# Performance work log

Measured on AMD Instinct MI355X. Metric: run time of the kernel, lower is better.

Reference implementation:

```python
import jax, jax.numpy as jnp
import numpy as np

S, B, E = 4096, 2, 1024
H = 8
WIN = 256  # one-sided window w; band width = 2*w+1


def _band_scores(q, k_pad, seq_len, band):
    # q: (B,S,H,D), k_pad: (B,S+2w,H,D). Returns (B,S,H,band) banded QK^T.
    def f(o):
        ks = jax.lax.dynamic_slice_in_dim(k_pad, o, seq_len, axis=1)
        return jnp.einsum('bshd,bshd->bsh', q, ks)
    s = jax.lax.map(f, jnp.arange(band))  # (band,B,S,H)
    return jnp.moveaxis(s, 0, -1)          # (B,S,H,band)


def _band_av(probs, v_pad, seq_len, band):
    # probs: (B,S,H,band), v_pad: (B,S+2w,H,D) zero-padded (out-of-range keys
    # contribute zero vectors, matching diagonaled_mm's internal masking).
    bsz, _, heads, _ = probs.shape
    d = v_pad.shape[-1]
    def body(carry, o):
        vs = jax.lax.dynamic_slice_in_dim(v_pad, o, seq_len, axis=1)
        p = jax.lax.dynamic_slice_in_dim(probs, o, 1, axis=3)  # (B,S,H,1)
        return carry + p * vs, None
    init = jnp.zeros((bsz, seq_len, heads, d), probs.dtype)
    out, _ = jax.lax.scan(body, init, jnp.arange(band))
    return out


def setup_inputs() -> dict:
    key = jax.random.key(0)
    ks = jax.random.split(key, 7)
    val = jax.random.normal(ks[0], (S, B, E), dtype=jnp.float32)
    Wq = jax.random.normal(ks[1], (E, E), dtype=jnp.float32) * 0.02
    bq = jax.random.normal(ks[2], (E,), dtype=jnp.float32) * 0.02
    Wk = jax.random.normal(ks[3], (E, E), dtype=jnp.float32) * 0.02
    bk = jax.random.normal(ks[4], (E,), dtype=jnp.float32) * 0.02
    Wv = jax.random.normal(ks[5], (E, E), dtype=jnp.float32) * 0.02
    bv = jax.random.normal(ks[6], (E,), dtype=jnp.float32) * 0.02
    return {"val": val, "Wq": Wq, "bq": bq, "Wk": Wk, "bk": bk, "Wv": Wv, "bv": bv}


def reference(val, Wq, bq, Wk, bk, Wv, bv):
    seq_len, bsz, embed = val.shape
    heads, w = H, WIN
    d = embed // heads
    band = 2 * w + 1
    x = jnp.swapaxes(val, 0, 1)  # (B,S,E), matches val.transpose(0,1)
    scale = 1.0 / np.sqrt(d)
    q = (x @ Wq.T + bq) * scale
    k = x @ Wk.T + bk
    v = x @ Wv.T + bv
    # Faithful to torch: .view(seq_len, bsz, H, D) on a (bsz, seq_len, E)
    # contiguous tensor reinterprets memory (a scramble when B != S), then
    # transpose(0,1). jnp.reshape on row-major matches torch .view exactly.
    mq = jnp.swapaxes(q.reshape(seq_len, bsz, heads, d), 0, 1)  # (B,S,H,D)
    mk = jnp.swapaxes(k.reshape(seq_len, bsz, heads, d), 0, 1)
    mv = jnp.swapaxes(v.reshape(seq_len, bsz, heads, d), 0, 1)
    k_pad = jnp.pad(mk, ((0, 0), (w, w), (0, 0), (0, 0)))  # zero pad => padding=0 scores
    v_pad = jnp.pad(mv, ((0, 0), (w, w), (0, 0), (0, 0)))
    scores = _band_scores(mq, k_pad, seq_len, band)  # (B,S,H,2w+1)
    # No masking before softmax (faithful: padding=0 entries enter softmax as 0)
    probs = jax.nn.softmax(scores, axis=-1)
    # dropout in eval mode (training=False) is identity
    attn = _band_av(probs, v_pad, seq_len, band)  # (B,S,H,D)
    out = jnp.swapaxes(attn, 0, 1).reshape(seq_len, bsz, embed)
    return out
```

## Files before the change

### kernel.cpp

```cpp
#include <hip/hip_runtime.h>
#include <stdint.h>

#define SEQ   4096
#define EMB   1024
#define HD    128
#define WIN   256
#define MROWS 8192

typedef unsigned short u16;
typedef unsigned long long u64;
typedef __bf16 v8bf  __attribute__((ext_vector_type(8)));
typedef float  v4f   __attribute__((ext_vector_type(4)));
typedef u16    v8u16 __attribute__((ext_vector_type(8)));

__device__ __forceinline__ u16 f2bf(float f) {
  uint32_t u = __builtin_bit_cast(uint32_t, f);
  u += 0x7FFFu + ((u >> 16) & 1u);
  return (u16)(u >> 16);
}
__device__ __forceinline__ void gl_lds16(const u16* g, u16* l) {
  __builtin_amdgcn_global_load_lds((const __attribute__((address_space(1))) void*)g,
                                   (__attribute__((address_space(3))) void*)l,
                                   16, 0, 0);
}

__global__ __launch_bounds__(256)
void cvt_f32_bf16(const float* __restrict__ val,
                  const float* __restrict__ Wq,
                  const float* __restrict__ Wk,
                  const float* __restrict__ Wv,
                  u16* __restrict__ valbf, u16* __restrict__ Wbf)
{
  const int seg = blockIdx.y;
  const float* src; u16* dst; int nblk;
  if (seg == 0)      { src = val; dst = valbf;              nblk = 4096; }
  else if (seg == 1) { src = Wq;  dst = Wbf;                nblk = 512;  }
  else if (seg == 2) { src = Wk;  dst = Wbf + (1u << 20);   nblk = 512;  }
  else               { src = Wv;  dst = Wbf + (2u << 20);   nblk = 512;  }
  if ((int)blockIdx.x >= nblk) return;
  const int t = blockIdx.x * 256 + threadIdx.x;
  float4 a = ((const float4*)src)[2 * t];
  float4 b = ((const float4*)src)[2 * t + 1];
  v8u16 o;
  o[0] = f2bf(a.x); o[1] = f2bf(a.y); o[2] = f2bf(a.z); o[3] = f2bf(a.w);
  o[4] = f2bf(b.x); o[5] = f2bf(b.y); o[6] = f2bf(b.z); o[7] = f2bf(b.w);
  ((v8u16*)dst)[t] = o;
}

__global__ __launch_bounds__(256, 3)
void qkv_gemm(const u16* __restrict__ valbf, const u16* __restrict__ Wbf,
              const float* __restrict__ bq, const float* __restrict__ bk,
              const float* __restrict__ bv,
              u16* __restrict__ Qb, u16* __restrict__ Kb, u16* __restrict__ VTg)
{
  __shared__ __align__(16) u16 As[128 * 64];
  __shared__ __align__(16) u16 Bs[128 * 64];

  const int tid  = threadIdx.x;
  const int lane = tid & 63;
  const int w    = tid >> 6;
  const int quad = lane >> 4;
  const int lq   = lane & 15;
  const int wm   = w >> 1, wn = w & 1;

  const int bn = blockIdx.x;
  const int bm = blockIdx.y;

  const int seg = bn >> 3;
  const u16*   Wsel = Wbf + (size_t)seg * EMB * EMB;
  const float* bsel = seg == 0 ? bq : (seg == 1 ? bk : bv);
  const int nseg0 = (bn & 7) * 128;

  const u16* arow[4];
  const u16* brow[4];
#pragma unroll
  for (int call = 0; call < 4; ++call) {
    int c  = call * 256 + w * 64 + lane;
    int m  = c >> 3;
    int qs = c & 7;
    int q  = qs ^ (m & 7);
    int a2 = bm * 128 + m;
    int aa = 2 * (a2 & 4095) + (a2 >> 12);
    int grow = (aa & 4095) * 2 + (aa >> 12);
    arow[call] = valbf + (size_t)grow * EMB + q * 8;
    int n = nseg0 + m;
    brow[call] = Wsel + (size_t)n * EMB + q * 8;
  }

  v4f acc[4][4];
#pragma unroll
  for (int mt = 0; mt < 4; ++mt)
#pragma unroll
    for (int nt = 0; nt < 4; ++nt) acc[mt][nt] = (v4f){0.f, 0.f, 0.f, 0.f};

#pragma unroll 1
  for (int kt = 0; kt < 16; ++kt) {
    const int k0 = kt * 64;
    __syncthreads();
#pragma unroll
    for (int call = 0; call < 4; ++call) {
      gl_lds16(arow[call] + k0, &As[(call * 256 + w * 64) * 8]);
      gl_lds16(brow[call] + k0, &Bs[(call * 256 + w * 64) * 8]);
    }
    __syncthreads();
#pragma unroll
    for (int ks = 0; ks < 2; ++ks) {
      v8bf afr[4], bfr[4];
      const int qa = ks * 4 + quad;
#pragma unroll
      for (int mt = 0; mt < 4; ++mt) {
        int m = wm * 64 + mt * 16 + lq;
        afr[mt] = *(const v8bf*)&As[(m * 8 + (qa ^ (m & 7))) * 8];
      }
#pragma unroll
      for (int nt = 0; nt < 4; ++nt) {
        int n = wn * 64 + nt * 16 + lq;
        bfr[nt] = *(const v8bf*)&Bs[(n * 8 + (qa ^ (n & 7))) * 8];
      }
#pragma unroll
      for (int mt = 0; mt < 4; ++mt)
#pragma unroll
        for (int nt = 0; nt < 4; ++nt)
          acc[mt][nt] = __builtin_amdgcn_mfma_f32_16x16x32_bf16(afr[mt], bfr[nt], acc[mt][nt], 0, 0, 0);
    }
  }

  const float scale = 0.08838834764831845f;
  float bias[4];
#pragma unroll
  for (int nt = 0; nt < 4; ++nt)
    bias[nt] = bsel[nseg0 + wn * 64 + nt * 16 + lq];

  if (seg == 2) {
    const int h  = bn & 7;
    const int bp = bm >> 5;
    const int s0 = (bm & 31) * 128;
#pragma unroll
    for (int mt = 0; mt < 4; ++mt) {
      int mb = wm * 64 + mt * 16 + quad * 4;
#pragma unroll
      for (int nt = 0; nt < 4; ++nt) {
        int n = wn * 64 + nt * 16 + lq;
        u64 pk = 0;
#pragma unroll
        for (int r = 0; r < 4; ++r)
          pk |= (u64)f2bf(acc[mt][nt][r] + bias[nt]) << (16 * r);
        *(u64*)&VTg[((size_t)(bp * 8 + h) * HD + n) * SEQ + s0 + mb] = pk;
      }
    }
  } else {
    u16* Osel = (seg == 0) ? Qb : Kb;
#pragma unroll
    for (int mt = 0; mt < 4; ++mt) {
      int rbase = bm * 128 + wm * 64 + mt * 16 + quad * 4;
#pragma unroll
      for (int nt = 0; nt < 4; ++nt) {
        int ncol = nseg0 + wn * 64 + nt * 16 + lq;
#pragma unroll
        for (int r = 0; r < 4; ++r) {
          float v = acc[mt][nt][r] + bias[nt];
          if (seg == 0) v *= scale;
          Osel[(size_t)(rbase + r) * EMB + ncol] = f2bf(v);
        }
      }
    }
  }
}

__global__ __launch_bounds__(256, 2)
void local_attn(const u16* __restrict__ Qb, const u16* __restrict__ Kb,
                const u16* __restrict__ VTg, float* __restrict__ out)
{
  __shared__ __align__(16) u16 sVT[2][128 * 64];
  __shared__ __align__(16) u16 sP[64 * 72];

  const int tid  = threadIdx.x;
  const int lane = tid & 63;
  const int w    = tid >> 6;
  const int quad = lane >> 4;
  const int lq   = lane & 15;

  const int bh = blockIdx.x;
  const int q0 = blockIdx.y * 64;
  const int bp = bh >> 3;
  const int h  = bh & 7;
  const size_t rowbase = (size_t)bp * SEQ;

  v8bf qf[4];
  {
    const u16* qrow = Qb + (rowbase + q0 + w * 16 + lq) * EMB + h * HD;
#pragma unroll
    for (int ks = 0; ks < 4; ++ks)
      qf[ks] = *(const v8bf*)(qrow + ks * 32 + quad * 8);
  }

  v4f oacc[8];
#pragma unroll
  for (int dt = 0; dt < 8; ++dt) oacc[dt] = (v4f){0.f, 0.f, 0.f, 0.f};
  float ls[4] = {0.f, 0.f, 0.f, 0.f};

  const int jlo = (q0 - WIN > 0) ? q0 - WIN : 0;
  const int jhi = (q0 + 64 + WIN < SEQ) ? q0 + 64 + WIN : SEQ;
  const int nit = (jhi - jlo) >> 6;

  auto stageVT = [&](int kb, int p) {
#pragma unroll
    for (int call = 0; call < 4; ++call) {
      int c = (w * 4 + call) * 64 + lane;
      int d = c >> 3, slot = c & 7;
      int q = slot ^ (d & 7);
      gl_lds16(VTg + ((size_t)bh * HD + d) * SEQ + kb + q * 8,
               &sVT[p][(w * 4 + call) * 512]);
    }
  };

  stageVT(jlo, 0);
  v8bf kfc[4][4];
#pragma unroll
  for (int ks = 0; ks < 4; ++ks)
#pragma unroll
    for (int nt = 0; nt < 4; ++nt)
      kfc[ks][nt] = *(const v8bf*)(Kb + (rowbase + jlo + nt * 16 + lq) * EMB
                                   + h * HD + ks * 32 + quad * 8);

  for (int it = 0; it < nit; ++it) {
    const int p  = it & 1;
    const int kb = jlo + it * 64;
    __syncthreads();
    if (it + 1 < nit) stageVT(kb + 64, p ^ 1);
    const int kbn = (it + 1 < nit) ? kb + 64 : jlo;

    v4f sfr[4];
#pragma unroll
    for (int nt = 0; nt < 4; ++nt) sfr[nt] = (v4f){0.f, 0.f, 0.f, 0.f};
#pragma unroll
    for (int ks = 0; ks < 4; ++ks) {
#pragma unroll
      for (int nt = 0; nt < 4; ++nt)
        sfr[nt] = __builtin_amdgcn_mfma_f32_16x16x32_bf16(qf[ks], kfc[ks][nt], sfr[nt], 0, 0, 0);
#pragma unroll
      for (int nt = 0; nt < 4; ++nt)
        kfc[ks][nt] = *(const v8bf*)(Kb + (rowbase + kbn + nt * 16 + lq) * EMB
                                     + h * HD + ks * 32 + quad * 8);
    }

#pragma unroll
    for (int nt = 0; nt < 4; ++nt) {
      int j = kb + nt * 16 + lq;
#pragma unroll
      for (int r = 0; r < 4; ++r) {
        int sr = q0 + w * 16 + quad * 4 + r;
        int dd = j - sr;
        float pv = (dd <= WIN && dd >= -WIN) ? __expf(sfr[nt][r]) : 0.f;
        ls[r] += pv;
        sP[(w * 16 + quad * 4 + r) * 72 + nt * 16 + lq] = f2bf(pv);
      }
    }

#pragma unroll
    for (int ks = 0; ks < 2; ++ks) {
      v8bf pf = *(const v8bf*)&sP[(w * 16 + lq) * 72 + ks * 32 + quad * 8];
      const int qn = ks * 4 + quad;
#pragma unroll
      for (int dt = 0; dt < 8; ++dt) {
        int d = dt * 16 + lq;
        v8bf vf = *(const v8bf*)&sVT[p][(d * 8 + (qn ^ (d & 7))) * 8];
        oacc[dt] = __builtin_amdgcn_mfma_f32_16x16x32_bf16(pf, vf, oacc[dt], 0, 0, 0);
      }
    }
  }

  float lrow[4];
#pragma unroll
  for (int r = 0; r < 4; ++r) {
    float t = ls[r];
#pragma unroll
    for (int off = 1; off < 16; off <<= 1) t += __shfl_xor(t, off);
    int sr = q0 + w * 16 + quad * 4 + r;
    int npl = WIN - sr;             if (npl < 0) npl = 0;
    int npr = sr - (SEQ - 1 - WIN); if (npr < 0) npr = 0;
    lrow[r] = t + (float)(npl + npr);
  }
#pragma unroll
  for (int dt = 0; dt < 8; ++dt) {
#pragma unroll
    for (int r = 0; r < 4; ++r) {
      int sr = q0 + w * 16 + quad * 4 + r;
      out[(size_t)(2 * sr + bp) * EMB + h * HD + dt * 16 + lq] = oacc[dt][r] / lrow[r];
    }
  }
}

extern "C" void kernel_launch(void* const* d_in, const int* in_sizes, int n_in,
                              void* d_out, int out_size, void* d_ws, size_t ws_size,
                              hipStream_t stream) {
  const float* val = (const float*)d_in[0];
  const float* bq  = (const float*)d_in[2];
  const float* bk  = (const float*)d_in[4];
  const float* bv  = (const float*)d_in[6];
  float* out = (float*)d_out;

  u16* valbf = (u16*)d_ws;
  u16* Wbf   = valbf + (size_t)MROWS * EMB;
  u16* Qb    = Wbf + (size_t)3 * EMB * EMB;
  u16* Kb    = Qb + (size_t)MROWS * EMB;
  u16* VTg   = Kb + (size_t)MROWS * EMB;

  hipLaunchKernelGGL(cvt_f32_bf16, dim3(4096, 4), dim3(256), 0, stream,
                     val, (const float*)d_in[1], (const float*)d_in[3],
                     (const float*)d_in[5], valbf, Wbf);
  hipLaunchKernelGGL(qkv_gemm, dim3(24, 64), dim3(256), 0, stream,
                     valbf, Wbf, bq, bk, bv, Qb, Kb, VTg);
  hipLaunchKernelGGL(local_attn, dim3(16, 64), dim3(256), 0, stream,
                     Qb, Kb, VTg, out);
}
```

Measured before the change: 234.0 us.

## Load V fragments directly from global, drop shared V staging and barriers

The attention kernel no longer stages V^T tiles into shared memory with async global-to-LDS copies and double buffering. Each wave now loads its V fragments straight from global memory into registers and keeps its own per-wave P buffer, which removes the block-wide __syncthreads. The band mask is also applied only on the two edge key blocks, and the QKV GEMM grid is transposed so the M tiles vary fastest. This cuts LDS use and synchronisation, but each of the four waves now fetches the same V tile from global/L2 and register pressure rises.

```diff
diff --git a/kernel.cpp b/kernel.cpp
--- a/kernel.cpp
+++ b/kernel.cpp
@@ -63,8 +63,8 @@
   const int lq   = lane & 15;
   const int wm   = w >> 1, wn = w & 1;
 
-  const int bn = blockIdx.x;
-  const int bm = blockIdx.y;
+  const int bm = blockIdx.x;
+  const int bn = blockIdx.y;
 
   const int seg = bn >> 3;
   const u16*   Wsel = Wbf + (size_t)seg * EMB * EMB;
@@ -171,8 +171,7 @@
 void local_attn(const u16* __restrict__ Qb, const u16* __restrict__ Kb,
                 const u16* __restrict__ VTg, float* __restrict__ out)
 {
-  __shared__ __align__(16) u16 sVT[2][128 * 64];
-  __shared__ __align__(16) u16 sP[64 * 72];
+  __shared__ __align__(16) u16 sP[4][16 * 72];
 
   const int tid  = threadIdx.x;
   const int lane = tid & 63;
@@ -203,31 +202,20 @@
   const int jhi = (q0 + 64 + WIN < SEQ) ? q0 + 64 + WIN : SEQ;
   const int nit = (jhi - jlo) >> 6;
 
-  auto stageVT = [&](int kb, int p) {
-#pragma unroll
-    for (int call = 0; call < 4; ++call) {
-      int c = (w * 4 + call) * 64 + lane;
-      int d = c >> 3, slot = c & 7;
-      int q = slot ^ (d & 7);
-      gl_lds16(VTg + ((size_t)bh * HD + d) * SEQ + kb + q * 8,
-               &sVT[p][(w * 4 + call) * 512]);
-    }
-  };
-
-  stageVT(jlo, 0);
+  const u16* Kbase = Kb + rowbase * EMB + h * HD;
+  const u16* Vbase = VTg + (size_t)bh * HD * SEQ;
+
   v8bf kfc[4][4];
 #pragma unroll
   for (int ks = 0; ks < 4; ++ks)
 #pragma unroll
     for (int nt = 0; nt < 4; ++nt)
-      kfc[ks][nt] = *(const v8bf*)(Kb + (rowbase + jlo + nt * 16 + lq) * EMB
-                                   + h * HD + ks * 32 + quad * 8);
-
+      kfc[ks][nt] = *(const v8bf*)(Kbase + (size_t)(jlo + nt * 16 + lq) * EMB
+                                   + ks * 32 + quad * 8);
+
+#pragma unroll 1
   for (int it = 0; it < nit; ++it) {
-    const int p  = it & 1;
-    const int kb = jlo + it * 64;
-    __syncthreads();
-    if (it + 1 < nit) stageVT(kb + 64, p ^ 1);
+    const int kb  = jlo + it * 64;
     const int kbn = (it + 1 < nit) ? kb + 64 : jlo;
 
     v4f sfr[4];
@@ -240,33 +228,41 @@
         sfr[nt] = __builtin_amdgcn_mfma_f32_16x16x32_bf16(qf[ks], kfc[ks][nt], sfr[nt], 0, 0, 0);
 #pragma unroll
       for (int nt = 0; nt < 4; ++nt)
-        kfc[ks][nt] = *(const v8bf*)(Kb + (rowbase + kbn + nt * 16 + lq) * EMB
-                                     + h * HD + ks * 32 + quad * 8);
-    }
-
+        kfc[ks][nt] = *(const v8bf*)(Kbase + (size_t)(kbn + nt * 16 + lq) * EMB
+                                     + ks * 32 + quad * 8);
+    }
+
+    v8bf vfc[2][8];
+#pragma unroll
+    for (int kv = 0; kv < 2; ++kv)
+#pragma unroll
+      for (int dt = 0; dt < 8; ++dt)
+        vfc[kv][dt] = *(const v8bf*)(Vbase + (size_t)(dt * 16 + lq) * SEQ
+                                     + kb + kv * 32 + quad * 8);
+
+    const bool need_mask = (kb == q0 - 256) || (kb == q0 + 256);
 #pragma unroll
     for (int nt = 0; nt < 4; ++nt) {
-      int j = kb + nt * 16 + lq;
 #pragma unroll
       for (int r = 0; r < 4; ++r) {
-        int sr = q0 + w * 16 + quad * 4 + r;
-        int dd = j - sr;
-        float pv = (dd <= WIN && dd >= -WIN) ? __expf(sfr[nt][r]) : 0.f;
+        float pv = __expf(sfr[nt][r]);
+        if (need_mask) {
+          int j  = kb + nt * 16 + lq;
+          int sr = q0 + w * 16 + quad * 4 + r;
+          int dd = j - sr;
+          pv = (dd <= WIN && dd >= -WIN) ? pv : 0.f;
+        }
         ls[r] += pv;
-        sP[(w * 16 + quad * 4 + r) * 72 + nt * 16 + lq] = f2bf(pv);
-      }
-    }
-
-#pragma unroll
-    for (int ks = 0; ks < 2; ++ks) {
-      v8bf pf = *(const v8bf*)&sP[(w * 16 + lq) * 72 + ks * 32 + quad * 8];
-      const int qn = ks * 4 + quad;
-#pragma unroll
-      for (int dt = 0; dt < 8; ++dt) {
-        int d = dt * 16 + lq;
-        v8bf vf = *(const v8bf*)&sVT[p][(d * 8 + (qn ^ (d & 7))) * 8];
-        oacc[dt] = __builtin_amdgcn_mfma_f32_16x16x32_bf16(pf, vf, oacc[dt], 0, 0, 0);
-      }
+        sP[w][(quad * 4 + r) * 72 + nt * 16 + lq] = f2bf(pv);
+      }
+    }
+
+#pragma unroll
+    for (int kv = 0; kv < 2; ++kv) {
+      v8bf pf = *(const v8bf*)&sP[w][lq * 72 + kv * 32 + quad * 8];
+#pragma unroll
+      for (int dt = 0; dt < 8; ++dt)
+        oacc[dt] = __builtin_amdgcn_mfma_f32_16x16x32_bf16(pf, vfc[kv][dt], oacc[dt], 0, 0, 0);
     }
   }
 
@@ -309,7 +305,7 @@
   hipLaunchKernelGGL(cvt_f32_bf16, dim3(4096, 4), dim3(256), 0, stream,
                      val, (const float*)d_in[1], (const float*)d_in[3],
                      (const float*)d_in[5], valbf, Wbf);
-  hipLaunchKernelGGL(qkv_gemm, dim3(24, 64), dim3(256), 0, stream,
+  hipLaunchKernelGGL(qkv_gemm, dim3(64, 24), dim3(256), 0, stream,
                      valbf, Wbf, bq, bk, bv, Qb, Kb, VTg);
   hipLaunchKernelGGL(local_attn, dim3(16, 64), dim3(256), 0, stream,
                      Qb, Kb, VTg, out);
```

After: 282.7 us. 1.21x slower.
